# Kernel optimization log

Measured on AMD Instinct MI355X. Metric: run time of the kernel, lower is better.

Reference implementation:

```python
import jax, jax.numpy as jnp
import numpy as np

B = 1024
IN_H, IN_W = 128, 128
KH, KW = 10, 10
SH, SW = 5, 5
PH, PW = 2, 2
HP, WP = IN_H + 2 * PH, IN_W + 2 * PW          # padded dims: 132, 132
NKH = (IN_H - KH + 2 * PH) // SH + 1            # 25
NKW = (IN_W - KW + 2 * PW) // SW + 1            # 25
NK = NKH * NKW                                  # 625


def _build_weight_matrix(kernel_weights):
    """kernel_weights: [NK, KH, KW] -> sparse-structured dense [HP*WP, NK].
    Faithful to LocallyConnected2dV2._create_weight_matrix, vectorized."""
    i = jnp.arange(NK)
    start_i = (i // NKW) * SH                   # [NK]
    start_j = (i % NKW) * SW                    # [NK]
    # flat row index for each (kernel, k, l) tap in padded image
    rows = ((start_i[:, None, None] + jnp.arange(KH)[None, :, None]) * WP
            + start_j[:, None, None] + jnp.arange(KW)[None, None, :])  # [NK,KH,KW]
    rows = rows.reshape(NK, KH * KW)
    cols = i[:, None]                           # [NK,1] broadcasts over taps
    W = jnp.zeros((HP * WP, NK), dtype=kernel_weights.dtype)
    return W.at[rows, cols].set(kernel_weights.reshape(NK, KH * KW))


def setup_inputs() -> dict:
    key = jax.random.key(0)
    kx, kw, kb = jax.random.split(key, 3)
    x = jax.random.normal(kx, (B, IN_H, IN_W), dtype=jnp.float32)
    kernel_weights = jax.random.normal(kw, (NK, KH, KW), dtype=jnp.float32)
    W = _build_weight_matrix(kernel_weights)    # [HP*WP, NK]
    bias = jax.random.normal(kb, (NKH, NKW), dtype=jnp.float32)
    return {"x": x, "W": W, "bias": bias}


def reference(x, W, bias):
    # zero-pad spatial dims, flatten, dense GEMM against sparse-structured W
    xp = jnp.pad(x, ((0, 0), (PH, PH), (PW, PW)))          # [B,HP,WP]
    xf = xp.reshape(x.shape[0], HP * WP)                   # [B,HP*WP]
    out = xf @ W                                           # [B,NK]
    out = out.reshape(x.shape[0], NKH, NKW)
    return out + bias
```

## Files before the change

### kernel.cpp

```cpp
#include <hip/hip_runtime.h>

constexpr int BATCH = 1024;
constexpr int H     = 128;
constexpr int Wd    = 128;
constexpr int WPAD  = 132;
constexpr int KH    = 10;
constexpr int KW    = 10;
constexpr int STR   = 5;
constexpr int NKH   = 25;
constexpr int NKW   = 25;
constexpr int NK    = NKH * NKW;
constexpr int KSZ   = KH * KW;

constexpr int IMGS  = 2;
constexpr int ITERS = 4;
constexpr int IPB   = IMGS * ITERS;
constexpr int GGRP  = BATCH / IPB;

__global__ void gather_weights(const float* __restrict__ W, float* __restrict__ wg) {
    int t = blockIdx.x * blockDim.x + threadIdx.x;
    if (t >= NK * KSZ) return;
    int k  = t / KSZ, i = t % KSZ;
    int di = i / KW,  dj = i % KW;
    int ki = k / NKW, kj = k % NKW;
    int row = (ki * STR + di) * WPAD + (kj * STR + dj);
    wg[t] = W[row * NK + k];
}

template <bool USE_WG>
__global__ __launch_bounds__(256)
void lc2d_kernel(const float* __restrict__ x,
                 const float* __restrict__ wg,
                 const float* __restrict__ Wfull,
                 const float* __restrict__ bias,
                 float* __restrict__ out) {
    __shared__ float xs[IMGS][KH][WPAD];
    __shared__ float part[IMGS][NKW * KH + 2];

    const int ki  = blockIdx.x % NKH;
    const int g   = blockIdx.x / NKH;
    const int tid = threadIdx.x;
    const int kj  = tid / KH;
    const int di  = tid % KH;

    float wr[KW];
    if (tid < NKW * KH) {
        const int k = ki * NKW + kj;
        if (USE_WG) {
#pragma unroll
            for (int dj = 0; dj < KW; ++dj)
                wr[dj] = wg[k * KSZ + di * KW + dj];
        } else {
#pragma unroll
            for (int dj = 0; dj < KW; ++dj) {
                int row = (ki * STR + di) * WPAD + (kj * STR + dj);
                wr[dj] = Wfull[row * NK + k];
            }
        }
    }
    float bia = 0.f;
    if (tid < IMGS * NKW) bia = bias[ki * NKW + tid % NKW];

    if (tid < IMGS * KH * 4) {
        const int img = tid / (KH * 4);
        const int j   = tid % (KH * 4);
        const int r   = j / 4, c = j % 4;
        xs[img][r][(c < 2) ? c : (128 + c)] = 0.f;
    }

    const int r0 = ki * STR - 2;

    for (int it = 0; it < ITERS; ++it) {
        const int b0 = g * IPB + it * IMGS;

        for (int i = tid; i < IMGS * KH * 32; i += 256) {
            const int img = i / (KH * 32);
            const int j   = i % (KH * 32);
            const int r   = j / 32, c4 = j % 32;
            const int rg  = r0 + r;
            float4 v = make_float4(0.f, 0.f, 0.f, 0.f);
            if (rg >= 0 && rg < H)
                v = reinterpret_cast<const float4*>(
                        x + (long)(b0 + img) * (H * Wd) + rg * Wd)[c4];
            float* dst = &xs[img][r][2 + c4 * 4];
            dst[0] = v.x; dst[1] = v.y; dst[2] = v.z; dst[3] = v.w;
        }
        __syncthreads();

        if (tid < NKW * KH) {
#pragma unroll
            for (int img = 0; img < IMGS; ++img) {
                float s = 0.f;
                const float* xr = &xs[img][di][kj * STR];
#pragma unroll
                for (int dj = 0; dj < KW; ++dj)
                    s += xr[dj] * wr[dj];
                part[img][tid] = s;
            }
        }
        __syncthreads();

        if (tid < IMGS * NKW) {
            const int img = tid / NKW, kj2 = tid % NKW;
            float s = 0.f;
#pragma unroll
            for (int j2 = 0; j2 < KH; ++j2)
                s += part[img][kj2 * KH + j2];
            out[(long)(b0 + img) * NK + ki * NKW + kj2] = s + bia;
        }
    }
}

extern "C" void kernel_launch(void* const* d_in, const int* in_sizes, int n_in,
                              void* d_out, int out_size, void* d_ws, size_t ws_size,
                              hipStream_t stream) {
    const float* x    = (const float*)d_in[0];
    const float* W    = (const float*)d_in[1];
    const float* bias = (const float*)d_in[2];
    float* out = (float*)d_out;

    const dim3 grid(NKH * GGRP);
    if (ws_size >= (size_t)NK * KSZ * sizeof(float)) {
        float* wg = (float*)d_ws;
        gather_weights<<<(NK * KSZ + 255) / 256, 256, 0, stream>>>(W, wg);
        lc2d_kernel<true><<<grid, 256, 0, stream>>>(x, wg, W, bias, out);
    } else {
        lc2d_kernel<false><<<grid, 256, 0, stream>>>(x, nullptr, W, bias, out);
    }
}
```

Measured before the change: 132.5 us.

## Register-block five kernels per thread and process five images per step

Each thread now holds 50 weights (five adjacent kernels for one row) and computes five dot products from a 36-float window read with float4 shared-memory loads. Each iteration handles 5 images instead of 2, and the weight workspace is re-laid out so every thread can load its weights with vector loads. The staging pass now also writes the zero padding, rows are padded to 136 floats, and the partial-sum reduction uses vector reads. Together these aim to cut shared-memory traffic and per-image overhead, at the cost of higher register pressure, ragged tail handling because 1024 is not a multiple of 15, and a switch on alignment.

```diff
diff --git a/kernel.cpp b/kernel.cpp
--- a/kernel.cpp
+++ b/kernel.cpp
@@ -12,102 +12,161 @@
 constexpr int NK    = NKH * NKW;
 constexpr int KSZ   = KH * KW;
 
-constexpr int IMGS  = 2;
-constexpr int ITERS = 4;
+constexpr int IMGS  = 5;
+constexpr int ITERS = 3;
 constexpr int IPB   = IMGS * ITERS;
-constexpr int GGRP  = BATCH / IPB;
+constexpr int NGRP  = (BATCH + IPB - 1) / IPB;
+constexpr int XST   = 136;
+constexpr int WG2_STRIDE = 52;
+constexpr int WG2_ROWS   = NKH * 5 * KH;
+constexpr int WG2_FLOATS = WG2_ROWS * WG2_STRIDE;
 
-__global__ void gather_weights(const float* __restrict__ W, float* __restrict__ wg) {
+__global__ void gather_w(const float* __restrict__ W, float* __restrict__ wg2) {
     int t = blockIdx.x * blockDim.x + threadIdx.x;
-    if (t >= NK * KSZ) return;
-    int k  = t / KSZ, i = t % KSZ;
-    int di = i / KW,  dj = i % KW;
-    int ki = k / NKW, kj = k % NKW;
+    if (t >= WG2_ROWS * 50) return;
+    int grp = t / 50, e = t % 50;
+    int kl = e / 10, dj = e % 10;
+    int di = grp % 10, gg = (grp / 10) % 5, ki = grp / 50;
+    int kj = 5 * gg + kl;
+    int k  = ki * NKW + kj;
     int row = (ki * STR + di) * WPAD + (kj * STR + dj);
-    wg[t] = W[row * NK + k];
+    wg2[grp * WG2_STRIDE + e] = W[row * NK + k];
+}
+
+template <int O>
+__device__ __forceinline__ void dot50(const float* __restrict__ f,
+                                      const float* __restrict__ w,
+                                      float* __restrict__ s) {
+#pragma unroll
+    for (int kl = 0; kl < 5; ++kl) {
+        float a = 0.f;
+#pragma unroll
+        for (int dj = 0; dj < 10; ++dj)
+            a += f[O + 5 * kl + dj] * w[kl * 10 + dj];
+        s[kl] = a;
+    }
 }
 
 template <bool USE_WG>
-__global__ __launch_bounds__(256)
+__global__ __launch_bounds__(256, 4)
 void lc2d_kernel(const float* __restrict__ x,
-                 const float* __restrict__ wg,
+                 const float* __restrict__ wg2,
                  const float* __restrict__ Wfull,
                  const float* __restrict__ bias,
                  float* __restrict__ out) {
-    __shared__ float xs[IMGS][KH][WPAD];
-    __shared__ float part[IMGS][NKW * KH + 2];
+    __shared__ float xs[IMGS][KH][XST];
+    __shared__ float part[IMGS][NKW][12];
 
-    const int ki  = blockIdx.x % NKH;
-    const int g   = blockIdx.x / NKH;
+    const int bid = blockIdx.x;
+    const int ki  = bid % NKH;
+    const int grp = bid / NKH;
     const int tid = threadIdx.x;
-    const int kj  = tid / KH;
-    const int di  = tid % KH;
 
-    float wr[KW];
-    if (tid < NKW * KH) {
-        const int k = ki * NKW + kj;
+    const bool active = tid < IMGS * KH * 5;
+    const int img = tid / 50;
+    const int di  = (tid / 5) % 10;
+    const int g   = tid % 5;
+
+    const int r0 = ki * STR - 2;
+    const int rg = r0 + di;
+    const bool rowok = (rg >= 0);
+
+    float w[50];
+    if (active) {
         if (USE_WG) {
+            const float4* src = reinterpret_cast<const float4*>(
+                wg2 + (size_t)(((ki * 5 + g) * 10 + di) * WG2_STRIDE));
+            float tmp[52];
 #pragma unroll
-            for (int dj = 0; dj < KW; ++dj)
-                wr[dj] = wg[k * KSZ + di * KW + dj];
+            for (int q = 0; q < 13; ++q) {
+                float4 v = src[q];
+                tmp[4 * q] = v.x; tmp[4 * q + 1] = v.y;
+                tmp[4 * q + 2] = v.z; tmp[4 * q + 3] = v.w;
+            }
+#pragma unroll
+            for (int i = 0; i < 50; ++i) w[i] = tmp[i];
         } else {
 #pragma unroll
-            for (int dj = 0; dj < KW; ++dj) {
-                int row = (ki * STR + di) * WPAD + (kj * STR + dj);
-                wr[dj] = Wfull[row * NK + k];
+            for (int kl = 0; kl < 5; ++kl) {
+                const int kj = 5 * g + kl, kcol = ki * NKW + kj;
+#pragma unroll
+                for (int dj = 0; dj < 10; ++dj) {
+                    int row = (ki * STR + di) * WPAD + kj * STR + dj;
+                    w[kl * 10 + dj] = Wfull[row * NK + kcol];
+                }
             }
         }
     }
-    float bia = 0.f;
-    if (tid < IMGS * NKW) bia = bias[ki * NKW + tid % NKW];
 
-    if (tid < IMGS * KH * 4) {
-        const int img = tid / (KH * 4);
-        const int j   = tid % (KH * 4);
-        const int r   = j / 4, c = j % 4;
-        xs[img][r][(c < 2) ? c : (128 + c)] = 0.f;
+    float bval = 0.f;
+    int himg = 0, hkj = 0;
+    if (tid < IMGS * NKW) {
+        himg = tid / NKW; hkj = tid % NKW;
+        bval = bias[ki * NKW + hkj];
     }
 
-    const int r0 = ki * STR - 2;
+    const int sb = (25 * g + 2) & ~3;
+    const int o  = (25 * g + 2) & 3;
 
-    for (int it = 0; it < ITERS; ++it) {
-        const int b0 = g * IPB + it * IMGS;
+    auto stage = [&](int it) {
+        if (!active) return;
+        const int b = grp * IPB + it * IMGS + img;
+        const bool bok = (b < BATCH) && rowok;
+        const float* xr = x + ((size_t)b << 14) + ((size_t)rg << 7);
+        float* dst = &xs[img][di][0];
+#pragma unroll
+        for (int jj = 0; jj < 7; ++jj) {
+            const int q = g * 7 + jj;
+            if (q < 33) {
+                float4 v = make_float4(0.f, 0.f, 0.f, 0.f);
+                if (q > 0 && bok)
+                    v = *reinterpret_cast<const float4*>(xr + 4 * q - 4);
+                *reinterpret_cast<float4*>(dst + 4 * q) = v;
+            }
+        }
+    };
 
-        for (int i = tid; i < IMGS * KH * 32; i += 256) {
-            const int img = i / (KH * 32);
-            const int j   = i % (KH * 32);
-            const int r   = j / 32, c4 = j % 32;
-            const int rg  = r0 + r;
-            float4 v = make_float4(0.f, 0.f, 0.f, 0.f);
-            if (rg >= 0 && rg < H)
-                v = reinterpret_cast<const float4*>(
-                        x + (long)(b0 + img) * (H * Wd) + rg * Wd)[c4];
-            float* dst = &xs[img][r][2 + c4 * 4];
-            dst[0] = v.x; dst[1] = v.y; dst[2] = v.z; dst[3] = v.w;
-        }
-        __syncthreads();
+    stage(0);
+    __syncthreads();
 
-        if (tid < NKW * KH) {
+    for (int it = 0;; ++it) {
+        if (active) {
+            float f[36];
+            const float* src = &xs[img][di][sb];
 #pragma unroll
-            for (int img = 0; img < IMGS; ++img) {
-                float s = 0.f;
-                const float* xr = &xs[img][di][kj * STR];
+            for (int q = 0; q < 9; ++q) {
+                float4 v = *reinterpret_cast<const float4*>(src + 4 * q);
+                f[4 * q] = v.x; f[4 * q + 1] = v.y;
+                f[4 * q + 2] = v.z; f[4 * q + 3] = v.w;
+            }
+            float s[5];
+            switch (o) {
+                case 0: dot50<0>(f, w, s); break;
+                case 1: dot50<1>(f, w, s); break;
+                case 2: dot50<2>(f, w, s); break;
+                default: dot50<3>(f, w, s); break;
+            }
 #pragma unroll
-                for (int dj = 0; dj < KW; ++dj)
-                    s += xr[dj] * wr[dj];
-                part[img][tid] = s;
-            }
+            for (int kl = 0; kl < 5; ++kl)
+                part[img][5 * g + kl][di] = s[kl];
         }
         __syncthreads();
 
         if (tid < IMGS * NKW) {
-            const int img = tid / NKW, kj2 = tid % NKW;
-            float s = 0.f;
-#pragma unroll
-            for (int j2 = 0; j2 < KH; ++j2)
-                s += part[img][kj2 * KH + j2];
-            out[(long)(b0 + img) * NK + ki * NKW + kj2] = s + bia;
+            const int b = grp * IPB + it * IMGS + himg;
+            if (b < BATCH) {
+                const float* p = &part[himg][hkj][0];
+                float4 a = *reinterpret_cast<const float4*>(p);
+                float4 c = *reinterpret_cast<const float4*>(p + 4);
+                float2 e = *reinterpret_cast<const float2*>(p + 8);
+                float ssum = ((a.x + a.y) + (a.z + a.w))
+                           + ((c.x + c.y) + (c.z + c.w)) + (e.x + e.y);
+                out[(size_t)b * NK + ki * NKW + hkj] = ssum + bval;
+            }
         }
+        if (it + 1 == ITERS) break;
+        stage(it + 1);
+        __syncthreads();
     }
 }
 
@@ -119,11 +178,11 @@
     const float* bias = (const float*)d_in[2];
     float* out = (float*)d_out;
 
-    const dim3 grid(NKH * GGRP);
-    if (ws_size >= (size_t)NK * KSZ * sizeof(float)) {
-        float* wg = (float*)d_ws;
-        gather_weights<<<(NK * KSZ + 255) / 256, 256, 0, stream>>>(W, wg);
-        lc2d_kernel<true><<<grid, 256, 0, stream>>>(x, wg, W, bias, out);
+    const dim3 grid(NKH * NGRP);
+    if (ws_size >= (size_t)WG2_FLOATS * sizeof(float)) {
+        float* wg2 = (float*)d_ws;
+        gather_w<<<(WG2_ROWS * 50 + 255) / 256, 256, 0, stream>>>(W, wg2);
+        lc2d_kernel<true><<<grid, 256, 0, stream>>>(x, wg2, W, bias, out);
     } else {
         lc2d_kernel<false><<<grid, 256, 0, stream>>>(x, nullptr, W, bias, out);
     }
```

Result: slower. 153.5 us (+15.9%).
